# Kernel tuning notes

Hardware: AMD Instinct MI355X
Metric: run time of the kernel (lower is better)

Reference implementation:

```python
import jax, jax.numpy as jnp
import numpy as np

BETA = 0.95
THRESHOLD = 1.0
NUM_STEPS = 255

# snntorch Heaviside spike with ATan surrogate gradient (alpha=2):
# forward: (x > 0), backward: g / (1 + (pi*x)^2)
@jax.custom_vjp
def heaviside_atan(x):
    return (x > 0).astype(x.dtype)

def _h_fwd(x):
    return heaviside_atan(x), x

def _h_bwd(x, g):
    return (g / (1.0 + (jnp.pi * x) ** 2),)

heaviside_atan.defvjp(_h_fwd, _h_bwd)


def setup_inputs() -> dict:
    key = jax.random.key(0)
    k1, k2 = jax.random.split(key)
    x = jax.random.normal(k1, (65536, 784), dtype=jnp.float32)
    W = jax.random.normal(k2, (1, 784), dtype=jnp.float32) * 0.035  # ~1/sqrt(784)
    return {"x": x, "W": W}


def reference(x, W):
    # fc(x) is identical every step -> compute once (same math as the loop)
    cur = x @ W.T  # [B, 1]
    mem0 = jnp.zeros_like(cur)

    def step(mem, _):
        # snntorch Leaky, reset_mechanism='zero':
        # reset computed from PREVIOUS membrane, then decay+input, zeroed on reset
        reset = heaviside_atan(mem - THRESHOLD)
        mem_new = (BETA * mem + cur) * (1.0 - reset)
        spk = heaviside_atan(mem_new - THRESHOLD)
        return mem_new, (spk, mem_new)

    _, (spk_rec, mem_rec) = jax.lax.scan(step, mem0, None, length=NUM_STEPS)
    # spk_rec, mem_rec: [NUM_STEPS, B, 1] -- matches torch.stack(dim=0)
    return spk_rec, mem_rec
```

## Files before the change

kernel.cpp:

```cpp
#include <hip/hip_runtime.h>


#define NROWS   65536
#define DIM     784
#define STEPS   255
#define BETA    0.95
#define CHUNK   32
#define NCHUNK  8

__global__ __launch_bounds__(256) void snn_matvec(const float* __restrict__ x,
                                                  const float* __restrict__ W,
                                                  double* __restrict__ cur) {
    const int lane = threadIdx.x & 63;
    const long long row = (long long)blockIdx.x * 4 + (threadIdx.x >> 6);

    const float4* __restrict__ W4 = (const float4*)W;
    const float4* __restrict__ xr = (const float4*)(x + row * DIM);

    float4 a0 = xr[lane];
    float4 a1 = xr[lane + 64];
    float4 a2 = xr[lane + 128];
    float4 w0 = W4[lane];
    float4 w1 = W4[lane + 64];
    float4 w2 = W4[lane + 128];
    float4 a3 = make_float4(0.f, 0.f, 0.f, 0.f);
    float4 w3 = make_float4(0.f, 0.f, 0.f, 0.f);
    if (lane < 4) { a3 = xr[192 + lane]; w3 = W4[192 + lane]; }

    double s = (double)a0.x * (double)w0.x + (double)a0.y * (double)w0.y
             + (double)a0.z * (double)w0.z + (double)a0.w * (double)w0.w
             + (double)a1.x * (double)w1.x + (double)a1.y * (double)w1.y
             + (double)a1.z * (double)w1.z + (double)a1.w * (double)w1.w
             + (double)a2.x * (double)w2.x + (double)a2.y * (double)w2.y
             + (double)a2.z * (double)w2.z + (double)a2.w * (double)w2.w
             + (double)a3.x * (double)w3.x + (double)a3.y * (double)w3.y
             + (double)a3.z * (double)w3.z + (double)a3.w * (double)w3.w;

    #pragma unroll
    for (int off = 32; off > 0; off >>= 1)
        s += __shfl_down(s, off, 64);

    if (lane == 0) cur[row] = s;
}

__device__ __forceinline__ double snn_step(double mem, double cur) {
    return (mem > 1.0) ? 0.0 : fma(BETA, mem, cur);
}

__global__ __launch_bounds__(256) void snn_recur(const double* __restrict__ curBuf,
                                                 float* __restrict__ out) {
    const int rowBlocks = NROWS / 256;
    const int chunk = blockIdx.x / rowBlocks;
    const long long row = (long long)(blockIdx.x % rowBlocks) * 256 + threadIdx.x;

    const double cur = curBuf[row];
    double mem = 0.0;

    const int warm = CHUNK * chunk;
    #pragma unroll 4
    for (int i = 0; i < warm; ++i)
        mem = snn_step(mem, cur);

    const int nst = (chunk == NCHUNK - 1) ? (CHUNK - 1) : CHUNK;
    float* __restrict__ spkOut = out + (long long)warm * NROWS + row;
    float* __restrict__ memOut = out + (long long)(STEPS + warm) * NROWS + row;

    for (int i = 0; i < nst; ++i) {
        mem = snn_step(mem, cur);
        __builtin_nontemporal_store((mem > 1.0) ? 1.0f : 0.0f, spkOut);
        __builtin_nontemporal_store((float)mem, memOut);
        spkOut += NROWS;
        memOut += NROWS;
    }
}

extern "C" void kernel_launch(void* const* d_in, const int* in_sizes, int n_in,
                              void* d_out, int out_size, void* d_ws, size_t ws_size,
                              hipStream_t stream) {
    const float* x = (const float*)d_in[0];
    const float* W = (const float*)d_in[1];
    float* out = (float*)d_out;
    double* cur = (double*)d_ws;

    hipLaunchKernelGGL(snn_matvec, dim3(NROWS / 4), dim3(256), 0, stream, x, W, cur);
    hipLaunchKernelGGL(snn_recur, dim3((NROWS / 256) * NCHUNK), dim3(256), 0, stream,
                       cur, out);
}
```

Measured before the change: 314.4 us.

## Fuse matvec and recurrence into a single kernel with shared-memory currents

Merges the dot-product kernel and the recurrence kernel into one launch, where each block computes 64 row currents into shared memory and then each wave runs one 64-step time chunk. This removes the second launch and the global round trip of the current buffer. In exchange, each wave reduces 16 rows serially, which gives less memory parallelism in the load phase, and the chunking changes to 4 chunks of 64 steps with longer warmup loops.

```diff
diff --git a/kernel.cpp b/kernel.cpp
--- a/kernel.cpp
+++ b/kernel.cpp
@@ -5,55 +5,62 @@
 #define DIM     784
 #define STEPS   255
 #define BETA    0.95
-#define CHUNK   32
-#define NCHUNK  8
-
-__global__ __launch_bounds__(256) void snn_matvec(const float* __restrict__ x,
-                                                  const float* __restrict__ W,
-                                                  double* __restrict__ cur) {
-    const int lane = threadIdx.x & 63;
-    const long long row = (long long)blockIdx.x * 4 + (threadIdx.x >> 6);
-
-    const float4* __restrict__ W4 = (const float4*)W;
-    const float4* __restrict__ xr = (const float4*)(x + row * DIM);
-
-    float4 a0 = xr[lane];
-    float4 a1 = xr[lane + 64];
-    float4 a2 = xr[lane + 128];
-    float4 w0 = W4[lane];
-    float4 w1 = W4[lane + 64];
-    float4 w2 = W4[lane + 128];
-    float4 a3 = make_float4(0.f, 0.f, 0.f, 0.f);
-    float4 w3 = make_float4(0.f, 0.f, 0.f, 0.f);
-    if (lane < 4) { a3 = xr[192 + lane]; w3 = W4[192 + lane]; }
-
-    double s = (double)a0.x * (double)w0.x + (double)a0.y * (double)w0.y
-             + (double)a0.z * (double)w0.z + (double)a0.w * (double)w0.w
-             + (double)a1.x * (double)w1.x + (double)a1.y * (double)w1.y
-             + (double)a1.z * (double)w1.z + (double)a1.w * (double)w1.w
-             + (double)a2.x * (double)w2.x + (double)a2.y * (double)w2.y
-             + (double)a2.z * (double)w2.z + (double)a2.w * (double)w2.w
-             + (double)a3.x * (double)w3.x + (double)a3.y * (double)w3.y
-             + (double)a3.z * (double)w3.z + (double)a3.w * (double)w3.w;
-
-    #pragma unroll
-    for (int off = 32; off > 0; off >>= 1)
-        s += __shfl_down(s, off, 64);
-
-    if (lane == 0) cur[row] = s;
-}
+#define ROWS_PB 64
+#define CHUNK   64
+#define NCHUNK  4
 
 __device__ __forceinline__ double snn_step(double mem, double cur) {
     return (mem > 1.0) ? 0.0 : fma(BETA, mem, cur);
 }
 
-__global__ __launch_bounds__(256) void snn_recur(const double* __restrict__ curBuf,
+__global__ __launch_bounds__(256) void snn_fused(const float* __restrict__ x,
+                                                 const float* __restrict__ W,
                                                  float* __restrict__ out) {
-    const int rowBlocks = NROWS / 256;
-    const int chunk = blockIdx.x / rowBlocks;
-    const long long row = (long long)(blockIdx.x % rowBlocks) * 256 + threadIdx.x;
+    __shared__ double cur_s[ROWS_PB];
+    const int tid  = threadIdx.x;
+    const int lane = tid & 63;
+    const int wave = tid >> 6;
+    const long long rowBase = (long long)blockIdx.x * ROWS_PB;
 
-    const double cur = curBuf[row];
+    {
+        const float4* __restrict__ W4 = (const float4*)W;
+        const float4 w0 = W4[lane];
+        const float4 w1 = W4[lane + 64];
+        const float4 w2 = W4[lane + 128];
+        float4 w3 = make_float4(0.f, 0.f, 0.f, 0.f);
+        if (lane < 4) w3 = W4[192 + lane];
+
+        #pragma unroll 2
+        for (int r = 0; r < 16; ++r) {
+            const int rl = wave * 16 + r;
+            const float4* __restrict__ xr = (const float4*)(x + (rowBase + rl) * DIM);
+            float4 a0 = xr[lane];
+            float4 a1 = xr[lane + 64];
+            float4 a2 = xr[lane + 128];
+            float4 a3 = make_float4(0.f, 0.f, 0.f, 0.f);
+            if (lane < 4) a3 = xr[192 + lane];
+
+            double s = (double)a0.x * (double)w0.x + (double)a0.y * (double)w0.y
+                     + (double)a0.z * (double)w0.z + (double)a0.w * (double)w0.w
+                     + (double)a1.x * (double)w1.x + (double)a1.y * (double)w1.y
+                     + (double)a1.z * (double)w1.z + (double)a1.w * (double)w1.w
+                     + (double)a2.x * (double)w2.x + (double)a2.y * (double)w2.y
+                     + (double)a2.z * (double)w2.z + (double)a2.w * (double)w2.w
+                     + (double)a3.x * (double)w3.x + (double)a3.y * (double)w3.y
+                     + (double)a3.z * (double)w3.z + (double)a3.w * (double)w3.w;
+
+            #pragma unroll
+            for (int off = 32; off > 0; off >>= 1)
+                s += __shfl_down(s, off, 64);
+
+            if (lane == 0) cur_s[rl] = s;
+        }
+    }
+    __syncthreads();
+
+    const int chunk = wave;
+    const long long row = rowBase + lane;
+    const double cur = cur_s[lane];
     double mem = 0.0;
 
     const int warm = CHUNK * chunk;
@@ -80,9 +87,7 @@
     const float* x = (const float*)d_in[0];
     const float* W = (const float*)d_in[1];
     float* out = (float*)d_out;
-    double* cur = (double*)d_ws;
 
-    hipLaunchKernelGGL(snn_matvec, dim3(NROWS / 4), dim3(256), 0, stream, x, W, cur);
-    hipLaunchKernelGGL(snn_recur, dim3((NROWS / 256) * NCHUNK), dim3(256), 0, stream,
-                       cur, out);
+    hipLaunchKernelGGL(snn_fused, dim3(NROWS / ROWS_PB), dim3(256), 0, stream,
+                       x, W, out);
 }
```

Result: slower. 328.0 us (+4.3%).
